# Optimization experiments

Hardware: AMD Instinct MI355X
Metric: run time of the kernel (lower is better)

The kernel has to match this reference:

```python
import jax, jax.numpy as jnp
import numpy as np

EPS = 1e-5
TOP_K = 2


def setup_inputs() -> dict:
    key = jax.random.key(0)
    ks = jax.random.split(key, 6)
    T, H, F, E = 4096, 1024, 2816, 8
    scale = 0.02
    return {
        "hidden_states": jax.random.normal(ks[0], (T, H), dtype=jnp.float32),
        "ln_w": jnp.ones((H,), dtype=jnp.float32),
        "router_w": jax.random.normal(ks[1], (H, E), dtype=jnp.float32) * scale,
        "w_gate": jax.random.normal(ks[2], (E, H, F), dtype=jnp.float32) * scale,
        "w_up": jax.random.normal(ks[3], (E, H, F), dtype=jnp.float32) * scale,
        "w_down": jax.random.normal(ks[4], (E, F, H), dtype=jnp.float32) * scale,
    }


def reference(hidden_states, ln_w, router_w, w_gate, w_up, w_down):
    # RMSNorm (LlamaRMSNorm)
    var = jnp.mean(hidden_states * hidden_states, axis=-1, keepdims=True)
    x = hidden_states * jax.lax.rsqrt(var + EPS) * ln_w  # [T, H]

    # TopKRouter: softmax over experts, then top-k probs/indices
    logits = x @ router_w                     # [T, E]
    probs = jax.nn.softmax(logits, axis=-1)
    topk_p, topk_i = jax.lax.top_k(probs, TOP_K)  # [T, K]

    # Dense combine weights [T, E]: prob for routed experts, 0 otherwise
    T = x.shape[0]
    combine = jnp.zeros_like(probs).at[jnp.arange(T)[:, None], topk_i].add(topk_p)

    # Experts: Llama-style gated MLP (SwiGLU); loop over fixed small expert set
    out = jnp.zeros_like(x)
    for e in range(w_gate.shape[0]):
        h = jax.nn.silu(x @ w_gate[e]) * (x @ w_up[e])   # [T, F]
        out = out + combine[:, e:e + 1] * (h @ w_down[e])
    return out
```

## Files before the change

### kernel.cpp

```cpp
#include <hip/hip_runtime.h>

#define T_TOK 4096
#define H_DIM 1024
#define F_DIM 2816
#define E_NUM 8
#define EPSV 1e-5f

typedef unsigned short u16;
typedef __attribute__((ext_vector_type(8))) short bf16x8;
typedef __attribute__((ext_vector_type(4))) float f32x4;

__device__ __forceinline__ u16 f2bf(float f) {
  union { float f; unsigned u; } c; c.f = f;
  unsigned u = c.u;
  return (u16)((u + 0x7FFFu + ((u >> 16) & 1u)) >> 16);
}

__device__ __forceinline__ void llds16(const u16* g, u16* l) {
  __builtin_amdgcn_global_load_lds(
      (const __attribute__((address_space(1))) unsigned int*)g,
      (__attribute__((address_space(3))) unsigned int*)l, 16, 0, 0);
}

__global__ __launch_bounds__(256) void router_kernel(
    const float* __restrict__ hs, const float* __restrict__ lnw,
    const float* __restrict__ rw, u16* __restrict__ x_h,
    int* __restrict__ cnt, int* __restrict__ list,
    float* __restrict__ wcomb) {
  const int wave = threadIdx.x >> 6;
  const int lane = threadIdx.x & 63;
  const int t = blockIdx.x * 4 + wave;
  const float* row = hs + (size_t)t * H_DIM;

  float4 v[4];
  float ss = 0.f;
#pragma unroll
  for (int j = 0; j < 4; ++j) {
    v[j] = ((const float4*)row)[j * 64 + lane];
    ss += v[j].x * v[j].x + v[j].y * v[j].y + v[j].z * v[j].z + v[j].w * v[j].w;
  }
#pragma unroll
  for (int m = 32; m; m >>= 1) ss += __shfl_xor(ss, m, 64);
  const float inv = rsqrtf(ss * (1.0f / H_DIM) + EPSV);

  float lg[E_NUM];
#pragma unroll
  for (int e = 0; e < E_NUM; ++e) lg[e] = 0.f;

#pragma unroll
  for (int j = 0; j < 4; ++j) {
    const int idx = j * 64 + lane;
    const int h0 = idx * 4;
    float4 w4 = ((const float4*)lnw)[idx];
    float xv[4] = {v[j].x * inv * w4.x, v[j].y * inv * w4.y,
                   v[j].z * inv * w4.z, v[j].w * inv * w4.w};
    ushort4 xs;
    xs.x = f2bf(xv[0]); xs.y = f2bf(xv[1]); xs.z = f2bf(xv[2]); xs.w = f2bf(xv[3]);
    ((ushort4*)(x_h + (size_t)t * H_DIM))[idx] = xs;
#pragma unroll
    for (int q = 0; q < 4; ++q) {
      const float* rr = rw + (size_t)(h0 + q) * E_NUM;
      float4 a = ((const float4*)rr)[0];
      float4 b = ((const float4*)rr)[1];
      lg[0] += xv[q] * a.x; lg[1] += xv[q] * a.y;
      lg[2] += xv[q] * a.z; lg[3] += xv[q] * a.w;
      lg[4] += xv[q] * b.x; lg[5] += xv[q] * b.y;
      lg[6] += xv[q] * b.z; lg[7] += xv[q] * b.w;
    }
  }
#pragma unroll
  for (int e = 0; e < E_NUM; ++e)
#pragma unroll
    for (int m = 32; m; m >>= 1) lg[e] += __shfl_xor(lg[e], m, 64);

  if (lane == 0) {
    float mx = lg[0];
#pragma unroll
    for (int e = 1; e < E_NUM; ++e) mx = fmaxf(mx, lg[e]);
    float p[E_NUM], s = 0.f;
#pragma unroll
    for (int e = 0; e < E_NUM; ++e) { p[e] = __expf(lg[e] - mx); s += p[e]; }
    const float invs = 1.0f / s;
    int e1 = 0; float b1 = p[0];
#pragma unroll
    for (int e = 1; e < E_NUM; ++e) if (p[e] > b1) { b1 = p[e]; e1 = e; }
    int e2 = -1; float b2 = -1.f;
#pragma unroll
    for (int e = 0; e < E_NUM; ++e) if (e != e1 && p[e] > b2) { b2 = p[e]; e2 = e; }
    b1 *= invs; b2 *= invs;
    int p1 = atomicAdd(&cnt[e1], 1);
    list[e1 * T_TOK + p1] = t; wcomb[e1 * T_TOK + p1] = b1;
    int p2 = atomicAdd(&cnt[e2], 1);
    list[e2 * T_TOK + p2] = t; wcomb[e2 * T_TOK + p2] = b2;
  }
}

__global__ void offsets_kernel(const int* __restrict__ cnt, int* __restrict__ offs) {
  if (threadIdx.x == 0) {
    int s = 0;
    for (int e = 0; e < E_NUM; ++e) { offs[e] = s; s += cnt[e]; }
  }
}

#define TPW 5632
__global__ __launch_bounds__(256) void transpose_cvt_all(
    const float* __restrict__ wg, const float* __restrict__ wu,
    const float* __restrict__ wd, u16* __restrict__ wgT,
    u16* __restrict__ wuT, u16* __restrict__ wdT) {
  __shared__ float tile[128][37];
  const int bx = blockIdx.x;
  const int which = bx / TPW;
  const int rem = bx - which * TPW;
  const int e = rem / 704;
  const int t = rem - e * 704;
  const float* in; u16* outp; int R, C, rt, ct;
  if (which == 0)      { in = wg; outp = wgT; R = H_DIM; C = F_DIM; rt = t / 88; ct = t - rt * 88; }
  else if (which == 1) { in = wu; outp = wuT; R = H_DIM; C = F_DIM; rt = t / 88; ct = t - rt * 88; }
  else                 { in = wd; outp = wdT; R = F_DIM; C = H_DIM; rt = t >> 5; ct = t & 31; }
  const size_t base = (size_t)e * R * C;
  const int r0 = rt * 128, c0 = ct * 32;
  const int tid = threadIdx.x;

  const int rr = tid >> 3, cq = tid & 7;
#pragma unroll
  for (int i = 0; i < 4; ++i) {
    float4 v = *(const float4*)(in + base + (size_t)(r0 + rr + 32 * i) * C + c0 + cq * 4);
    float* dst = &tile[rr + 32 * i][cq * 4];
    dst[0] = v.x; dst[1] = v.y; dst[2] = v.z; dst[3] = v.w;
  }
  __syncthreads();

  const int cc = tid >> 4, rq0 = tid & 15;
#pragma unroll
  for (int jj = 0; jj < 4; ++jj) {
    const int c = cc + 16 * (jj & 1);
    const int rq = rq0 + 16 * (jj >> 1);
    ushort4 o;
    o.x = f2bf(tile[rq * 4 + 0][c]);
    o.y = f2bf(tile[rq * 4 + 1][c]);
    o.z = f2bf(tile[rq * 4 + 2][c]);
    o.w = f2bf(tile[rq * 4 + 3][c]);
    *(ushort4*)(outp + base + (size_t)(c0 + c) * R + r0 + rq * 4) = o;
  }
}

__global__ __launch_bounds__(256) void gemm1_kernel(
    const u16* __restrict__ x_h, const u16* __restrict__ wgT,
    const u16* __restrict__ wuT, const int* __restrict__ cnt,
    const int* __restrict__ offs, const int* __restrict__ list,
    u16* __restrict__ hbuf) {
  const int e = blockIdx.z;
  const int n_e = cnt[e];
  const int rt = blockIdx.y;
  if (rt * 128 >= n_e) return;
  const int ft = blockIdx.x;

  __shared__ __align__(16) u16 As[2][128 * 64];
  __shared__ __align__(16) u16 Bgs[2][64 * 64];
  __shared__ __align__(16) u16 Bus[2][64 * 64];

  const int tid = threadIdx.x;
  const int wv = tid >> 6, lane = tid & 63;
  const int wm = wv >> 1, wn = wv & 1;
  const int lrow = lane & 15, quad = lane >> 4;
  const int srow = lane >> 3, schunk = lane & 7;

  const u16* agp[4];
#pragma unroll
  for (int i = 0; i < 4; ++i) {
    const int rl = wv * 32 + i * 8 + srow;
    int gr = rt * 128 + rl; if (gr >= n_e) gr = n_e - 1;
    const int tkn = list[e * T_TOK + gr];
    agp[i] = x_h + (size_t)tkn * H_DIM + ((schunk ^ (rl & 7)) << 3);
  }
  const size_t wb = ((size_t)e * F_DIM + (size_t)ft * 64) * H_DIM;
  const u16* bgp[2]; const u16* bup[2];
#pragma unroll
  for (int i = 0; i < 2; ++i) {
    const int r = wv * 16 + i * 8 + srow;
    const size_t g = wb + (size_t)r * H_DIM + ((schunk ^ (r & 7)) << 3);
    bgp[i] = wgT + g;
    bup[i] = wuT + g;
  }

  int aoff[4][2], boff[2][2];
#pragma unroll
  for (int tm = 0; tm < 4; ++tm) {
    const int row = wm * 64 + tm * 16 + lrow;
#pragma unroll
    for (int ks = 0; ks < 2; ++ks)
      aoff[tm][ks] = row * 64 + (((ks * 4 + quad) ^ (row & 7)) << 3);
  }
#pragma unroll
  for (int tn = 0; tn < 2; ++tn) {
    const int row = wn * 32 + tn * 16 + lrow;
#pragma unroll
    for (int ks = 0; ks < 2; ++ks)
      boff[tn][ks] = row * 64 + (((ks * 4 + quad) ^ (row & 7)) << 3);
  }

  f32x4 accg[4][2], accu[4][2];
#pragma unroll
  for (int i = 0; i < 4; ++i)
#pragma unroll
    for (int j = 0; j < 2; ++j) {
      accg[i][j] = f32x4{0.f, 0.f, 0.f, 0.f};
      accu[i][j] = f32x4{0.f, 0.f, 0.f, 0.f};
    }

  auto stage = [&](int b, int k0) {
#pragma unroll
    for (int i = 0; i < 4; ++i)
      llds16(agp[i] + k0, &As[b][(wv * 32 + i * 8) * 64]);
#pragma unroll
    for (int i = 0; i < 2; ++i) {
      llds16(bgp[i] + k0, &Bgs[b][(wv * 16 + i * 8) * 64]);
      llds16(bup[i] + k0, &Bus[b][(wv * 16 + i * 8) * 64]);
    }
  };
  auto compute = [&](int b) {
#pragma unroll
    for (int ks = 0; ks < 2; ++ks) {
      bf16x8 a[4], bg[2], bu[2];
#pragma unroll
      for (int tm = 0; tm < 4; ++tm) a[tm] = *(const bf16x8*)&As[b][aoff[tm][ks]];
#pragma unroll
      for (int tn = 0; tn < 2; ++tn) {
        bg[tn] = *(const bf16x8*)&Bgs[b][boff[tn][ks]];
        bu[tn] = *(const bf16x8*)&Bus[b][boff[tn][ks]];
      }
#pragma unroll
      for (int tm = 0; tm < 4; ++tm)
#pragma unroll
        for (int tn = 0; tn < 2; ++tn) {
          accg[tm][tn] = __builtin_amdgcn_mfma_f32_16x16x32_bf16(a[tm], bg[tn], accg[tm][tn], 0, 0, 0);
          accu[tm][tn] = __builtin_amdgcn_mfma_f32_16x16x32_bf16(a[tm], bu[tn], accu[tm][tn], 0, 0, 0);
        }
    }
  };

  stage(0, 0);
#pragma unroll 1
  for (int k0 = 0; k0 < H_DIM; k0 += 128) {
    const bool s1 = (k0 + 64) < H_DIM;
    if (s1) {
      stage(1, k0 + 64);
      asm volatile("s_waitcnt vmcnt(8)" ::: "memory");
    } else {
      asm volatile("s_waitcnt vmcnt(0)" ::: "memory");
    }
    __builtin_amdgcn_s_barrier();
    compute(0);
    __builtin_amdgcn_s_barrier();
    const bool s2 = (k0 + 128) < H_DIM;
    if (s2) {
      stage(0, k0 + 128);
      asm volatile("s_waitcnt vmcnt(8)" ::: "memory");
    } else {
      asm volatile("s_waitcnt vmcnt(0)" ::: "memory");
    }
    __builtin_amdgcn_s_barrier();
    compute(1);
    __builtin_amdgcn_s_barrier();
  }

  const int oe = offs[e];
#pragma unroll
  for (int tm = 0; tm < 4; ++tm) {
    const int lr0 = wm * 64 + tm * 16 + quad * 4;
#pragma unroll
    for (int rr = 0; rr < 4; ++rr) {
      const int gr = rt * 128 + lr0 + rr;
      if (gr < n_e) {
#pragma unroll
        for (int tn = 0; tn < 2; ++tn) {
          float g = accg[tm][tn][rr];
          float u = accu[tm][tn][rr];
          float hv = g / (1.0f + __expf(-g)) * u;
          int col = ft * 64 + wn * 32 + tn * 16 + lrow;
          hbuf[(size_t)(oe + gr) * F_DIM + col] = f2bf(hv);
        }
      }
    }
  }
}

__global__ __launch_bounds__(256) void gemm2_kernel(
    const u16* __restrict__ hbuf, const u16* __restrict__ wdT,
    const int* __restrict__ cnt, const int* __restrict__ offs,
    const float* __restrict__ wcomb, const int* __restrict__ list,
    float* __restrict__ out) {
  const int e = blockIdx.z;
  const int n_e = cnt[e];
  const int rt = blockIdx.y;
  if (rt * 128 >= n_e) return;
  const int nt = blockIdx.x;

  __shared__ __align__(16) u16 As[2][128 * 64];
  __shared__ __align__(16) u16 Bs[2][128 * 64];

  const int tid = threadIdx.x;
  const int oe = offs[e];
  const int wv = tid >> 6, lane = tid & 63;
  const int wm = wv >> 1, wn = wv & 1;
  const int lrow = lane & 15, quad = lane >> 4;
  const int srow = lane >> 3, schunk = lane & 7;

  const u16* agp[4];
#pragma unroll
  for (int i = 0; i < 4; ++i) {
    const int rl = wv * 32 + i * 8 + srow;
    int gr = rt * 128 + rl; if (gr >= n_e) gr = n_e - 1;
    agp[i] = hbuf + (size_t)(oe + gr) * F_DIM + ((schunk ^ (rl & 7)) << 3);
  }
  const size_t wb = ((size_t)e * H_DIM + (size_t)nt * 128) * F_DIM;
  const u16* bgp[4];
#pragma unroll
  for (int i = 0; i < 4; ++i) {
    const int r = wv * 32 + i * 8 + srow;
    bgp[i] = wdT + wb + (size_t)r * F_DIM + ((schunk ^ (r & 7)) << 3);
  }

  int aoff[4][2], boff[4][2];
#pragma unroll
  for (int tm = 0; tm < 4; ++tm) {
    const int row = wm * 64 + tm * 16 + lrow;
#pragma unroll
    for (int ks = 0; ks < 2; ++ks)
      aoff[tm][ks] = row * 64 + (((ks * 4 + quad) ^ (row & 7)) << 3);
  }
#pragma unroll
  for (int tn = 0; tn < 4; ++tn) {
    const int row = wn * 64 + tn * 16 + lrow;
#pragma unroll
    for (int ks = 0; ks < 2; ++ks)
      boff[tn][ks] = row * 64 + (((ks * 4 + quad) ^ (row & 7)) << 3);
  }

  f32x4 acc[4][4];
#pragma unroll
  for (int i = 0; i < 4; ++i)
#pragma unroll
    for (int j = 0; j < 4; ++j) acc[i][j] = f32x4{0.f, 0.f, 0.f, 0.f};

  auto stage = [&](int b, int k0) {
#pragma unroll
    for (int i = 0; i < 4; ++i) {
      llds16(agp[i] + k0, &As[b][(wv * 32 + i * 8) * 64]);
      llds16(bgp[i] + k0, &Bs[b][(wv * 32 + i * 8) * 64]);
    }
  };
  auto compute = [&](int b) {
#pragma unroll
    for (int ks = 0; ks < 2; ++ks) {
      bf16x8 a[4], bb[4];
#pragma unroll
      for (int tm = 0; tm < 4; ++tm) a[tm] = *(const bf16x8*)&As[b][aoff[tm][ks]];
#pragma unroll
      for (int tn = 0; tn < 4; ++tn) bb[tn] = *(const bf16x8*)&Bs[b][boff[tn][ks]];
#pragma unroll
      for (int tm = 0; tm < 4; ++tm)
#pragma unroll
        for (int tn = 0; tn < 4; ++tn)
          acc[tm][tn] = __builtin_amdgcn_mfma_f32_16x16x32_bf16(a[tm], bb[tn], acc[tm][tn], 0, 0, 0);
    }
  };

  stage(0, 0);
#pragma unroll 1
  for (int k0 = 0; k0 < F_DIM; k0 += 128) {
    const bool s1 = (k0 + 64) < F_DIM;
    if (s1) {
      stage(1, k0 + 64);
      asm volatile("s_waitcnt vmcnt(8)" ::: "memory");
    } else {
      asm volatile("s_waitcnt vmcnt(0)" ::: "memory");
    }
    __builtin_amdgcn_s_barrier();
    compute(0);
    __builtin_amdgcn_s_barrier();
    const bool s2 = (k0 + 128) < F_DIM;
    if (s2) {
      stage(0, k0 + 128);
      asm volatile("s_waitcnt vmcnt(8)" ::: "memory");
    } else {
      asm volatile("s_waitcnt vmcnt(0)" ::: "memory");
    }
    __builtin_amdgcn_s_barrier();
    compute(1);
    __builtin_amdgcn_s_barrier();
  }

#pragma unroll
  for (int tm = 0; tm < 4; ++tm) {
    const int lr0 = wm * 64 + tm * 16 + quad * 4;
#pragma unroll
    for (int rr = 0; rr < 4; ++rr) {
      const int gr = rt * 128 + lr0 + rr;
      if (gr < n_e) {
        const float cw = wcomb[e * T_TOK + gr];
        const int tkn = list[e * T_TOK + gr];
#pragma unroll
        for (int tn = 0; tn < 4; ++tn) {
          const int col = nt * 128 + wn * 64 + tn * 16 + lrow;
          atomicAdd(&out[(size_t)tkn * H_DIM + col], acc[tm][tn][rr] * cw);
        }
      }
    }
  }
}

extern "C" void kernel_launch(void* const* d_in, const int* in_sizes, int n_in,
                              void* d_out, int out_size, void* d_ws, size_t ws_size,
                              hipStream_t stream) {
  const float* hs  = (const float*)d_in[0];
  const float* lnw = (const float*)d_in[1];
  const float* rw  = (const float*)d_in[2];
  const float* wg  = (const float*)d_in[3];
  const float* wu  = (const float*)d_in[4];
  const float* wd  = (const float*)d_in[5];
  float* out = (float*)d_out;

  char* p = (char*)d_ws;
  const size_t SZ_XH = (size_t)T_TOK * H_DIM * 2;
  const size_t SZ_W  = (size_t)E_NUM * F_DIM * H_DIM * 2;
  const size_t SZ_HB = (size_t)T_TOK * 2 * F_DIM * 2;

  u16* x_h  = (u16*)p;   p += SZ_XH;
  u16* wgT  = (u16*)p;   p += SZ_W;
  u16* wuT  = (u16*)p;   p += SZ_W;
  u16* wdT  = (u16*)p;   p += SZ_W;
  u16* hbuf = (u16*)p;   p += SZ_HB;
  int* cnt  = (int*)p;   p += 256;
  int* offs = (int*)p;   p += 256;
  int* list = (int*)p;   p += (size_t)E_NUM * T_TOK * 4;
  float* wcomb = (float*)p; p += (size_t)E_NUM * T_TOK * 4;

  hipMemsetAsync(cnt, 0, 256, stream);
  hipMemsetAsync(out, 0, (size_t)T_TOK * H_DIM * 4, stream);
  router_kernel<<<T_TOK / 4, 256, 0, stream>>>(hs, lnw, rw, x_h, cnt, list, wcomb);
  offsets_kernel<<<1, 64, 0, stream>>>(cnt, offs);
  transpose_cvt_all<<<3 * TPW, 256, 0, stream>>>(wg, wu, wd, wgT, wuT, wdT);
  gemm1_kernel<<<dim3(F_DIM / 64, T_TOK / 128, E_NUM), 256, 0, stream>>>(x_h, wgT, wuT, cnt, offs, list, hbuf);
  gemm2_kernel<<<dim3(H_DIM / 128, T_TOK / 128, E_NUM), 256, 0, stream>>>(hbuf, wdT, cnt, offs, wcomb, list, out);
}
```

Measured before the change: 669.3 us.

## Enlarge gemm1 tile with interleaved gate/up B, replace atomics with combine pass

gemm1 now runs 512-thread blocks over a 256x128 tile with K-step 32. Gate and up weight rows are interleaved into a single B tile, so each wave issues one uniform MFMA grid and the A tile is reused across more columns. gemm2 no longer does fp32 atomicAdd into the output. It writes weighted per-slot contributions to a buffer, and a new combine kernel sums each token's two expert rows using slot indices recorded by the router. This removes the output memset and the atomic contention, at the cost of an extra fp32 buffer round trip, an extra launch, and possibly lower occupancy or more register pressure in gemm1.

```diff
diff --git a/kernel.cpp b/kernel.cpp
--- a/kernel.cpp
+++ b/kernel.cpp
@@ -26,7 +26,7 @@
     const float* __restrict__ hs, const float* __restrict__ lnw,
     const float* __restrict__ rw, u16* __restrict__ x_h,
     int* __restrict__ cnt, int* __restrict__ list,
-    float* __restrict__ wcomb) {
+    float* __restrict__ wcomb, int* __restrict__ slot) {
   const int wave = threadIdx.x >> 6;
   const int lane = threadIdx.x & 63;
   const int t = blockIdx.x * 4 + wave;
@@ -90,8 +90,10 @@
     b1 *= invs; b2 *= invs;
     int p1 = atomicAdd(&cnt[e1], 1);
     list[e1 * T_TOK + p1] = t; wcomb[e1 * T_TOK + p1] = b1;
+    slot[2 * t] = (e1 << 16) | p1;
     int p2 = atomicAdd(&cnt[e2], 1);
     list[e2 * T_TOK + p2] = t; wcomb[e2 * T_TOK + p2] = b2;
+    slot[2 * t + 1] = (e2 << 16) | p2;
   }
 }
 
@@ -144,7 +146,7 @@
   }
 }
 
-__global__ __launch_bounds__(256) void gemm1_kernel(
+__global__ __launch_bounds__(512, 2) void gemm1_kernel(
     const u16* __restrict__ x_h, const u16* __restrict__ wgT,
     const u16* __restrict__ wuT, const int* __restrict__ cnt,
     const int* __restrict__ offs, const int* __restrict__ list,
@@ -152,110 +154,83 @@
   const int e = blockIdx.z;
   const int n_e = cnt[e];
   const int rt = blockIdx.y;
-  if (rt * 128 >= n_e) return;
+  if (rt * 256 >= n_e) return;
   const int ft = blockIdx.x;
 
-  __shared__ __align__(16) u16 As[2][128 * 64];
-  __shared__ __align__(16) u16 Bgs[2][64 * 64];
-  __shared__ __align__(16) u16 Bus[2][64 * 64];
+  __shared__ __align__(16) u16 As[2][256 * 32];
+  __shared__ __align__(16) u16 Bs[2][256 * 32];
 
   const int tid = threadIdx.x;
   const int wv = tid >> 6, lane = tid & 63;
-  const int wm = wv >> 1, wn = wv & 1;
+  const int wm = wv >> 2, wn = wv & 3;
   const int lrow = lane & 15, quad = lane >> 4;
-  const int srow = lane >> 3, schunk = lane & 7;
-
-  const u16* agp[4];
-#pragma unroll
-  for (int i = 0; i < 4; ++i) {
-    const int rl = wv * 32 + i * 8 + srow;
-    int gr = rt * 128 + rl; if (gr >= n_e) gr = n_e - 1;
+
+  const u16* agp[2]; const u16* bgp[2];
+#pragma unroll
+  for (int i = 0; i < 2; ++i) {
+    const int r = (wv * 2 + i) * 16 + (lane >> 2);
+    const int chunk = (lane & 3) ^ ((r ^ (r >> 2)) & 3);
+    int gr = rt * 256 + r; if (gr >= n_e) gr = n_e - 1;
     const int tkn = list[e * T_TOK + gr];
-    agp[i] = x_h + (size_t)tkn * H_DIM + ((schunk ^ (rl & 7)) << 3);
-  }
-  const size_t wb = ((size_t)e * F_DIM + (size_t)ft * 64) * H_DIM;
-  const u16* bgp[2]; const u16* bup[2];
-#pragma unroll
-  for (int i = 0; i < 2; ++i) {
-    const int r = wv * 16 + i * 8 + srow;
-    const size_t g = wb + (size_t)r * H_DIM + ((schunk ^ (r & 7)) << 3);
-    bgp[i] = wgT + g;
-    bup[i] = wuT + g;
-  }
-
-  int aoff[4][2], boff[2][2];
-#pragma unroll
-  for (int tm = 0; tm < 4; ++tm) {
-    const int row = wm * 64 + tm * 16 + lrow;
-#pragma unroll
-    for (int ks = 0; ks < 2; ++ks)
-      aoff[tm][ks] = row * 64 + (((ks * 4 + quad) ^ (row & 7)) << 3);
-  }
-#pragma unroll
-  for (int tn = 0; tn < 2; ++tn) {
-    const int row = wn * 32 + tn * 16 + lrow;
-#pragma unroll
-    for (int ks = 0; ks < 2; ++ks)
-      boff[tn][ks] = row * 64 + (((ks * 4 + quad) ^ (row & 7)) << 3);
-  }
-
-  f32x4 accg[4][2], accu[4][2];
-#pragma unroll
-  for (int i = 0; i < 4; ++i)
-#pragma unroll
-    for (int j = 0; j < 2; ++j) {
-      accg[i][j] = f32x4{0.f, 0.f, 0.f, 0.f};
-      accu[i][j] = f32x4{0.f, 0.f, 0.f, 0.f};
-    }
+    agp[i] = x_h + (size_t)tkn * H_DIM + chunk * 8;
+    const int fcol = ft * 128 + ((r >> 5) << 4) + (r & 15);
+    const u16* src = ((r >> 4) & 1) ? wuT : wgT;
+    bgp[i] = src + ((size_t)e * F_DIM + fcol) * H_DIM + chunk * 8;
+  }
+
+  int aoff[8], boff[4];
+#pragma unroll
+  for (int tm = 0; tm < 8; ++tm) {
+    const int row = wm * 128 + tm * 16 + lrow;
+    aoff[tm] = row * 32 + (((quad ^ (row ^ (row >> 2))) & 3) << 3);
+  }
+#pragma unroll
+  for (int tn = 0; tn < 4; ++tn) {
+    const int row = wn * 64 + tn * 16 + lrow;
+    boff[tn] = row * 32 + (((quad ^ (row ^ (row >> 2))) & 3) << 3);
+  }
+
+  f32x4 acc[8][4];
+#pragma unroll
+  for (int i = 0; i < 8; ++i)
+#pragma unroll
+    for (int j = 0; j < 4; ++j) acc[i][j] = f32x4{0.f, 0.f, 0.f, 0.f};
 
   auto stage = [&](int b, int k0) {
 #pragma unroll
-    for (int i = 0; i < 4; ++i)
-      llds16(agp[i] + k0, &As[b][(wv * 32 + i * 8) * 64]);
-#pragma unroll
     for (int i = 0; i < 2; ++i) {
-      llds16(bgp[i] + k0, &Bgs[b][(wv * 16 + i * 8) * 64]);
-      llds16(bup[i] + k0, &Bus[b][(wv * 16 + i * 8) * 64]);
+      llds16(agp[i] + k0, &As[b][(wv * 2 + i) * 16 * 32]);
+      llds16(bgp[i] + k0, &Bs[b][(wv * 2 + i) * 16 * 32]);
     }
   };
   auto compute = [&](int b) {
-#pragma unroll
-    for (int ks = 0; ks < 2; ++ks) {
-      bf16x8 a[4], bg[2], bu[2];
-#pragma unroll
-      for (int tm = 0; tm < 4; ++tm) a[tm] = *(const bf16x8*)&As[b][aoff[tm][ks]];
-#pragma unroll
-      for (int tn = 0; tn < 2; ++tn) {
-        bg[tn] = *(const bf16x8*)&Bgs[b][boff[tn][ks]];
-        bu[tn] = *(const bf16x8*)&Bus[b][boff[tn][ks]];
-      }
-#pragma unroll
-      for (int tm = 0; tm < 4; ++tm)
-#pragma unroll
-        for (int tn = 0; tn < 2; ++tn) {
-          accg[tm][tn] = __builtin_amdgcn_mfma_f32_16x16x32_bf16(a[tm], bg[tn], accg[tm][tn], 0, 0, 0);
-          accu[tm][tn] = __builtin_amdgcn_mfma_f32_16x16x32_bf16(a[tm], bu[tn], accu[tm][tn], 0, 0, 0);
-        }
-    }
+    bf16x8 a[8], bb[4];
+#pragma unroll
+    for (int tm = 0; tm < 8; ++tm) a[tm] = *(const bf16x8*)&As[b][aoff[tm]];
+#pragma unroll
+    for (int tn = 0; tn < 4; ++tn) bb[tn] = *(const bf16x8*)&Bs[b][boff[tn]];
+#pragma unroll
+    for (int tm = 0; tm < 8; ++tm)
+#pragma unroll
+      for (int tn = 0; tn < 4; ++tn)
+        acc[tm][tn] = __builtin_amdgcn_mfma_f32_16x16x32_bf16(a[tm], bb[tn], acc[tm][tn], 0, 0, 0);
   };
 
   stage(0, 0);
 #pragma unroll 1
-  for (int k0 = 0; k0 < H_DIM; k0 += 128) {
-    const bool s1 = (k0 + 64) < H_DIM;
-    if (s1) {
-      stage(1, k0 + 64);
-      asm volatile("s_waitcnt vmcnt(8)" ::: "memory");
+  for (int k0 = 0; k0 < H_DIM; k0 += 64) {
+    if (k0 + 32 < H_DIM) {
+      stage(1, k0 + 32);
+      asm volatile("s_waitcnt vmcnt(4)" ::: "memory");
     } else {
       asm volatile("s_waitcnt vmcnt(0)" ::: "memory");
     }
     __builtin_amdgcn_s_barrier();
     compute(0);
     __builtin_amdgcn_s_barrier();
-    const bool s2 = (k0 + 128) < H_DIM;
-    if (s2) {
-      stage(0, k0 + 128);
-      asm volatile("s_waitcnt vmcnt(8)" ::: "memory");
+    if (k0 + 64 < H_DIM) {
+      stage(0, k0 + 64);
+      asm volatile("s_waitcnt vmcnt(4)" ::: "memory");
     } else {
       asm volatile("s_waitcnt vmcnt(0)" ::: "memory");
     }
@@ -266,18 +241,18 @@
 
   const int oe = offs[e];
 #pragma unroll
-  for (int tm = 0; tm < 4; ++tm) {
-    const int lr0 = wm * 64 + tm * 16 + quad * 4;
+  for (int tm = 0; tm < 8; ++tm) {
+    const int lr0 = wm * 128 + tm * 16 + quad * 4;
 #pragma unroll
     for (int rr = 0; rr < 4; ++rr) {
-      const int gr = rt * 128 + lr0 + rr;
+      const int gr = rt * 256 + lr0 + rr;
       if (gr < n_e) {
 #pragma unroll
-        for (int tn = 0; tn < 2; ++tn) {
-          float g = accg[tm][tn][rr];
-          float u = accu[tm][tn][rr];
+        for (int p = 0; p < 2; ++p) {
+          float g = acc[tm][2 * p][rr];
+          float u = acc[tm][2 * p + 1][rr];
           float hv = g / (1.0f + __expf(-g)) * u;
-          int col = ft * 64 + wn * 32 + tn * 16 + lrow;
+          const int col = ft * 128 + (wn * 2 + p) * 16 + lrow;
           hbuf[(size_t)(oe + gr) * F_DIM + col] = f2bf(hv);
         }
       }
@@ -288,8 +263,7 @@
 __global__ __launch_bounds__(256) void gemm2_kernel(
     const u16* __restrict__ hbuf, const u16* __restrict__ wdT,
     const int* __restrict__ cnt, const int* __restrict__ offs,
-    const float* __restrict__ wcomb, const int* __restrict__ list,
-    float* __restrict__ out) {
+    const float* __restrict__ wcomb, float* __restrict__ contrib) {
   const int e = blockIdx.z;
   const int n_e = cnt[e];
   const int rt = blockIdx.y;
@@ -399,15 +373,27 @@
       const int gr = rt * 128 + lr0 + rr;
       if (gr < n_e) {
         const float cw = wcomb[e * T_TOK + gr];
-        const int tkn = list[e * T_TOK + gr];
 #pragma unroll
         for (int tn = 0; tn < 4; ++tn) {
           const int col = nt * 128 + wn * 64 + tn * 16 + lrow;
-          atomicAdd(&out[(size_t)tkn * H_DIM + col], acc[tm][tn][rr] * cw);
+          contrib[(size_t)(oe + gr) * H_DIM + col] = acc[tm][tn][rr] * cw;
         }
       }
     }
   }
+}
+
+__global__ __launch_bounds__(256) void combine_kernel(
+    const float* __restrict__ contrib, const int* __restrict__ offs,
+    const int* __restrict__ slot, float* __restrict__ out) {
+  const int t = blockIdx.x;
+  const int s0 = slot[2 * t], s1 = slot[2 * t + 1];
+  const int r0 = offs[s0 >> 16] + (s0 & 0xFFFF);
+  const int r1 = offs[s1 >> 16] + (s1 & 0xFFFF);
+  float4 a = ((const float4*)(contrib + (size_t)r0 * H_DIM))[threadIdx.x];
+  float4 b = ((const float4*)(contrib + (size_t)r1 * H_DIM))[threadIdx.x];
+  float4 o = {a.x + b.x, a.y + b.y, a.z + b.z, a.w + b.w};
+  ((float4*)(out + (size_t)t * H_DIM))[threadIdx.x] = o;
 }
 
 extern "C" void kernel_launch(void* const* d_in, const int* in_sizes, int n_in,
@@ -425,22 +411,25 @@
   const size_t SZ_XH = (size_t)T_TOK * H_DIM * 2;
   const size_t SZ_W  = (size_t)E_NUM * F_DIM * H_DIM * 2;
   const size_t SZ_HB = (size_t)T_TOK * 2 * F_DIM * 2;
+  const size_t SZ_CT = (size_t)T_TOK * 2 * H_DIM * 4;
 
   u16* x_h  = (u16*)p;   p += SZ_XH;
   u16* wgT  = (u16*)p;   p += SZ_W;
   u16* wuT  = (u16*)p;   p += SZ_W;
   u16* wdT  = (u16*)p;   p += SZ_W;
   u16* hbuf = (u16*)p;   p += SZ_HB;
+  float* contrib = (float*)p; p += SZ_CT;
   int* cnt  = (int*)p;   p += 256;
   int* offs = (int*)p;   p += 256;
   int* list = (int*)p;   p += (size_t)E_NUM * T_TOK * 4;
   float* wcomb = (float*)p; p += (size_t)E_NUM * T_TOK * 4;
+  int* slot = (int*)p;   p += (size_t)T_TOK * 2 * 4;
 
   hipMemsetAsync(cnt, 0, 256, stream);
-  hipMemsetAsync(out, 0, (size_t)T_TOK * H_DIM * 4, stream);
-  router_kernel<<<T_TOK / 4, 256, 0, stream>>>(hs, lnw, rw, x_h, cnt, list, wcomb);
+  router_kernel<<<T_TOK / 4, 256, 0, stream>>>(hs, lnw, rw, x_h, cnt, list, wcomb, slot);
   offsets_kernel<<<1, 64, 0, stream>>>(cnt, offs);
   transpose_cvt_all<<<3 * TPW, 256, 0, stream>>>(wg, wu, wd, wgT, wuT, wdT);
-  gemm1_kernel<<<dim3(F_DIM / 64, T_TOK / 128, E_NUM), 256, 0, stream>>>(x_h, wgT, wuT, cnt, offs, list, hbuf);
-  gemm2_kernel<<<dim3(H_DIM / 128, T_TOK / 128, E_NUM), 256, 0, stream>>>(hbuf, wdT, cnt, offs, wcomb, list, out);
-}
+  gemm1_kernel<<<dim3(F_DIM / 128, T_TOK / 256, E_NUM), 512, 0, stream>>>(x_h, wgT, wuT, cnt, offs, list, hbuf);
+  gemm2_kernel<<<dim3(H_DIM / 128, T_TOK / 128, E_NUM), 256, 0, stream>>>(hbuf, wdT, cnt, offs, wcomb, contrib);
+  combine_kernel<<<T_TOK, 256, 0, stream>>>(contrib, offs, slot, out);
+}
```

Result: slower. 700.2 us (+4.6%).
